# Optimization experiments

Hardware: AMD Instinct MI355X
Metric: run time of the kernel (lower is better)

## Reference

```python
import jax, jax.numpy as jnp
import numpy as np

N_NODES = 200000
N_EDGES = 3200000
F_IN, HID, N_CLS = 128, 35, 10


def setup_inputs() -> dict:
    key = jax.random.key(0)
    k = jax.random.split(key, 5)
    x = jax.random.normal(k[0], (N_NODES, F_IN), dtype=jnp.float32)
    edge_index = jax.random.randint(k[1], (2, N_EDGES), 0, N_NODES, dtype=jnp.int64)
    W1 = jax.random.normal(k[2], (F_IN, HID), dtype=jnp.float32) / np.sqrt(F_IN)
    b1 = jnp.zeros((HID,), dtype=jnp.float32)
    W2 = jax.random.normal(k[3], (HID, N_CLS), dtype=jnp.float32) / np.sqrt(HID)
    b2 = jnp.zeros((N_CLS,), dtype=jnp.float32)
    return {"x": x, "edge_index": edge_index, "W1": W1, "b1": b1, "W2": W2, "b2": b2}


def _gcn_conv(x, W, b, row, col, norm, n_nodes):
    # GCNConv: linear transform, then normalized neighbor aggregation (scatter-add)
    h = x @ W                               # [N, d_out]
    msg = h[row] * norm[:, None]            # gather along edges, [E+N, d_out]
    agg = jax.ops.segment_sum(msg, col, num_segments=n_nodes)
    return agg + b


def reference(x, edge_index, W1, b1, W2, b2):
    n = x.shape[0]
    loop = jnp.arange(n, dtype=edge_index.dtype)
    row = jnp.concatenate([edge_index[0], loop])  # sources (+ self loops)
    col = jnp.concatenate([edge_index[1], loop])  # targets (+ self loops)
    deg = jax.ops.segment_sum(jnp.ones_like(col, dtype=x.dtype), col, num_segments=n)
    dinv = jnp.where(deg > 0, deg ** -0.5, 0.0)
    norm = dinv[row] * dinv[col]                  # D^{-1/2} A D^{-1/2} edge weights

    h = _gcn_conv(x, W1, b1, row, col, norm, n)
    h = jax.nn.relu(h)
    # F.dropout with training=self.training: identity at inference
    out = _gcn_conv(h, W2, b2, row, col, norm, n)
    return jax.nn.log_softmax(out, axis=1)
```

## Files before the change

kernel.cpp:

```cpp
#include <hip/hip_runtime.h>

#define NN    200000
#define F_IN  128
#define HID   35
#define LD1   36
#define LD2   12
#define LD2P  16
#define NCLS  10
#define NPB   256
#define NB    782
#define CAP   5120
#define EPT   32
#define NOE   0xFFFFFFFFu

static __device__ inline unsigned short f2bf(float f) {
    unsigned u = __float_as_uint(f);
    u = (u + 0x7FFFu + ((u >> 16) & 1u)) >> 16;
    return (unsigned short)u;
}
static __device__ inline unsigned pk2(float a, float b) {
    return (unsigned)f2bf(a) | ((unsigned)f2bf(b) << 16);
}
static __device__ inline float bflo(unsigned u) { return __uint_as_float(u << 16); }
static __device__ inline float bfhi(unsigned u) { return __uint_as_float(u & 0xFFFF0000u); }


__global__ void k_initcur(int* __restrict__ gcur) {
    int t = threadIdx.x;
    if (t < NB) gcur[t] = t * CAP;
}

__global__ __launch_bounds__(256)
void k_bucket(const int* __restrict__ row, const int* __restrict__ col, int E,
              int* __restrict__ gcur, unsigned* __restrict__ bkt) {
    __shared__ int hist[NB];
    __shared__ int basev[NB];
    int t = threadIdx.x;
    long e0 = (long)blockIdx.x * (256 * EPT);
    for (int i = t; i < NB; i += 256) hist[i] = 0;
    __syncthreads();
    int cols[EPT];
#pragma unroll
    for (int i = 0; i < EPT; ++i) {
        long e = e0 + (long)i * 256 + t;
        if (e < E) {
            int c = col[e];
            cols[i] = c;
            atomicAdd(&hist[c >> 8], 1);
        } else cols[i] = -1;
    }
    __syncthreads();
    for (int i = t; i < NB; i += 256) {
        int h = hist[i];
        basev[i] = (h > 0) ? atomicAdd(&gcur[i], h) : 0;
        hist[i] = 0;
    }
    __syncthreads();
#pragma unroll
    for (int i = 0; i < EPT; ++i) {
        int c = cols[i];
        if (c >= 0) {
            long e = e0 + (long)i * 256 + t;
            int r = row[e];
            int b = c >> 8;
            int pos = basev[b] + atomicAdd(&hist[b], 1);
            if (pos < NB * CAP) bkt[pos] = (unsigned)r | ((unsigned)(c & 255) << 18);
        }
    }
}

__global__ __launch_bounds__(256)
void k_sort(unsigned* __restrict__ bkt, const int* __restrict__ gcur,
            int* __restrict__ obeg, int* __restrict__ oend,
            float* __restrict__ dinv, int n) {
    __shared__ unsigned est[CAP];
    __shared__ int hist[NPB];
    __shared__ int cur[NPB];
    __shared__ int sc[NPB];
    int b = blockIdx.x, t = threadIdx.x;
    int ec = gcur[b] - b * CAP;
    if (ec > CAP) ec = CAP;
    unsigned* ep = bkt + (size_t)b * CAP;
    hist[t] = 0;
    __syncthreads();
    for (int e = t; e < ec; e += 256) {
        unsigned p = ep[e];
        est[e] = p;
        atomicAdd(&hist[p >> 18], 1);
    }
    __syncthreads();
    sc[t] = hist[t];
    __syncthreads();
    for (int d = 1; d < NPB; d <<= 1) {
        int add = (t >= d) ? sc[t - d] : 0;
        __syncthreads();
        sc[t] += add;
        __syncthreads();
    }
    int excl = sc[t] - hist[t];
    cur[t] = excl;
    int i = b * NPB + t;
    if (i < n) {
        obeg[i] = b * CAP + excl;
        oend[i] = b * CAP + excl + hist[t];
        dinv[i] = rsqrtf((float)(hist[t] + 1));
    }
    __syncthreads();
    for (int e = t; e < ec; e += 256) {
        unsigned p = est[e];
        int lc = p >> 18;
        int pos = atomicAdd(&cur[lc], 1);
        ep[pos] = p & 0x3FFFF;
    }
}


__global__ void k_gemm1(const float* __restrict__ x, const float* __restrict__ W1,
                        const float* __restrict__ dinv,
                        unsigned short* __restrict__ hs1A,
                        unsigned short* __restrict__ hs1B, int n) {
    int i = blockIdx.x * blockDim.x + threadIdx.x;
    if (i >= n) return;
    float acc[HID];
#pragma unroll
    for (int j = 0; j < HID; ++j) acc[j] = 0.f;
    const float4* xr = (const float4*)(x + (size_t)i * F_IN);
    for (int k4 = 0; k4 < F_IN / 4; ++k4) {
        float4 xv = xr[k4];
        const float* w = W1 + (size_t)(k4 * 4) * HID;
#pragma unroll
        for (int j = 0; j < HID; ++j)
            acc[j] += xv.x * w[j] + xv.y * w[HID + j] + xv.z * w[2 * HID + j] + xv.w * w[3 * HID + j];
    }
    float d = dinv[i];
    unsigned* oa = (unsigned*)(hs1A + (size_t)i * 32);
#pragma unroll
    for (int j = 0; j < 16; ++j) oa[j] = pk2(acc[2 * j] * d, acc[2 * j + 1] * d);
    unsigned* ob = (unsigned*)(hs1B + (size_t)i * 4);
    ob[0] = pk2(acc[32] * d, acc[33] * d);
    ob[1] = pk2(acc[34] * d, 0.f);
}

__global__ void k_agg1(const int* __restrict__ obeg, const int* __restrict__ oend,
                       const unsigned* __restrict__ srow,
                       const unsigned short* __restrict__ A,
                       const unsigned short* __restrict__ Bf,
                       float* __restrict__ acc1, int n) {
    int wv = (blockIdx.x * blockDim.x + threadIdx.x) >> 6;
    int lane = threadIdx.x & 63;
    int w0 = wv * 2, w1 = w0 + 1;
    if (w0 >= n) return;
    bool has1 = (w1 < n);
    int s = lane & 15;
    int g = lane >> 4;
    bool bl = (lane < 16);
    int beg0 = obeg[w0], end0 = oend[w0];
    int beg1 = has1 ? obeg[w1] : 0, end1 = has1 ? oend[w1] : 0;
    int nb0 = end0 - beg0, nb1 = end1 - beg1;
    int iters = max((nb0 + 15) >> 4, (nb1 + 15) >> 4);
    float p0a=0.f,p0b=0.f,p0c=0.f,p0d=0.f,p0e=0.f,p0f=0.f,p0g=0.f,p0h=0.f;
    float p1a=0.f,p1b=0.f,p1c=0.f,p1d=0.f,p1e=0.f,p1f=0.f,p1g=0.f,p1h=0.f;
    float q0a=0.f,q0b=0.f,q0c=0.f, q1a=0.f,q1b=0.f,q1c=0.f;
    int e0 = beg0 + s, e1 = beg1 + s;
    for (int it = 0; it < iters; ++it) {
        unsigned idx0 = (e0 < end0) ? srow[e0] : NOE;
        unsigned idx1 = (has1 && e1 < end1) ? srow[e1] : NOE;
        bool v0 = (idx0 != NOE), v1 = (idx1 != NOE);
        unsigned r0 = v0 ? idx0 : (unsigned)w0;
        unsigned r1 = v1 ? idx1 : (unsigned)w0;
        uint4 av0 = *(const uint4*)(A + ((size_t)r0 << 5) + (g << 3));
        uint4 av1 = *(const uint4*)(A + ((size_t)r1 << 5) + (g << 3));
        uint2 bv0 = make_uint2(0u, 0u), bv1 = make_uint2(0u, 0u);
        if (bl) {
            bv0 = *(const uint2*)(Bf + ((size_t)r0 << 2));
            bv1 = *(const uint2*)(Bf + ((size_t)r1 << 2));
        }
        if (v0) {
            p0a += bflo(av0.x); p0b += bfhi(av0.x);
            p0c += bflo(av0.y); p0d += bfhi(av0.y);
            p0e += bflo(av0.z); p0f += bfhi(av0.z);
            p0g += bflo(av0.w); p0h += bfhi(av0.w);
            if (bl) { q0a += bflo(bv0.x); q0b += bfhi(bv0.x); q0c += bflo(bv0.y); }
        }
        if (v1) {
            p1a += bflo(av1.x); p1b += bfhi(av1.x);
            p1c += bflo(av1.y); p1d += bfhi(av1.y);
            p1e += bflo(av1.z); p1f += bfhi(av1.z);
            p1g += bflo(av1.w); p1h += bfhi(av1.w);
            if (bl) { q1a += bflo(bv1.x); q1b += bfhi(bv1.x); q1c += bflo(bv1.y); }
        }
        e0 += 16; e1 += 16;
    }
#pragma unroll
    for (int d = 1; d < 16; d <<= 1) {
        p0a += __shfl_xor(p0a, d); p0b += __shfl_xor(p0b, d);
        p0c += __shfl_xor(p0c, d); p0d += __shfl_xor(p0d, d);
        p0e += __shfl_xor(p0e, d); p0f += __shfl_xor(p0f, d);
        p0g += __shfl_xor(p0g, d); p0h += __shfl_xor(p0h, d);
        p1a += __shfl_xor(p1a, d); p1b += __shfl_xor(p1b, d);
        p1c += __shfl_xor(p1c, d); p1d += __shfl_xor(p1d, d);
        p1e += __shfl_xor(p1e, d); p1f += __shfl_xor(p1f, d);
        p1g += __shfl_xor(p1g, d); p1h += __shfl_xor(p1h, d);
        q0a += __shfl_xor(q0a, d); q0b += __shfl_xor(q0b, d); q0c += __shfl_xor(q0c, d);
        q1a += __shfl_xor(q1a, d); q1b += __shfl_xor(q1b, d); q1c += __shfl_xor(q1c, d);
    }
    if (s == 0) {
        uint4 sv0 = *(const uint4*)(A + ((size_t)w0 << 5) + (g << 3));
        p0a += bflo(sv0.x); p0b += bfhi(sv0.x);
        p0c += bflo(sv0.y); p0d += bfhi(sv0.y);
        p0e += bflo(sv0.z); p0f += bfhi(sv0.z);
        p0g += bflo(sv0.w); p0h += bfhi(sv0.w);
        float* o0 = acc1 + (size_t)w0 * LD1 + (g << 3);
        *(float4*)o0       = make_float4(p0a, p0b, p0c, p0d);
        *(float4*)(o0 + 4) = make_float4(p0e, p0f, p0g, p0h);
        if (has1) {
            uint4 sv1 = *(const uint4*)(A + ((size_t)w1 << 5) + (g << 3));
            p1a += bflo(sv1.x); p1b += bfhi(sv1.x);
            p1c += bflo(sv1.y); p1d += bfhi(sv1.y);
            p1e += bflo(sv1.z); p1f += bfhi(sv1.z);
            p1g += bflo(sv1.w); p1h += bfhi(sv1.w);
            float* o1 = acc1 + (size_t)w1 * LD1 + (g << 3);
            *(float4*)o1       = make_float4(p1a, p1b, p1c, p1d);
            *(float4*)(o1 + 4) = make_float4(p1e, p1f, p1g, p1h);
        }
    }
    if (lane == 0) {
        uint2 sb0 = *(const uint2*)(Bf + ((size_t)w0 << 2));
        q0a += bflo(sb0.x); q0b += bfhi(sb0.x); q0c += bflo(sb0.y);
        *(float4*)(acc1 + (size_t)w0 * LD1 + 32) = make_float4(q0a, q0b, q0c, 0.f);
        if (has1) {
            uint2 sb1 = *(const uint2*)(Bf + ((size_t)w1 << 2));
            q1a += bflo(sb1.x); q1b += bfhi(sb1.x); q1c += bflo(sb1.y);
            *(float4*)(acc1 + (size_t)w1 * LD1 + 32) = make_float4(q1a, q1b, q1c, 0.f);
        }
    }
}


__global__ void k_layer2(const float* __restrict__ acc1, const float* __restrict__ dinv,
                         const float* __restrict__ b1, const float* __restrict__ W2,
                         unsigned short* __restrict__ hs2b, int n) {
    int i = blockIdx.x * blockDim.x + threadIdx.x;
    if (i >= n) return;
    float d = dinv[i];
    const float4* a = (const float4*)(acc1 + (size_t)i * LD1);
    float4 tq[9];
#pragma unroll
    for (int q = 0; q < 9; ++q) tq[q] = a[q];
    const float* tf = (const float*)tq;
    float h[HID];
#pragma unroll
    for (int k = 0; k < HID; ++k) {
        float v = tf[k] * d + b1[k];
        h[k] = v > 0.f ? v : 0.f;
    }
    float o[NCLS];
#pragma unroll
    for (int j = 0; j < NCLS; ++j) o[j] = 0.f;
#pragma unroll
    for (int k = 0; k < HID; ++k) {
#pragma unroll
        for (int j = 0; j < NCLS; ++j) o[j] += h[k] * W2[k * NCLS + j];
    }
    unsigned* dst = (unsigned*)(hs2b + (size_t)i * LD2P);
#pragma unroll
    for (int j = 0; j < 5; ++j) dst[j] = pk2(o[2 * j] * d, o[2 * j + 1] * d);
    dst[5] = 0u; dst[6] = 0u; dst[7] = 0u;
}

__global__ void k_agg2o(const int* __restrict__ obeg, const int* __restrict__ oend,
                        const unsigned* __restrict__ srow,
                        const unsigned short* __restrict__ H,
                        const float* __restrict__ dinv, const float* __restrict__ b2,
                        float* __restrict__ out, int n) {
    int wv = (blockIdx.x * blockDim.x + threadIdx.x) >> 6;
    int lane = threadIdx.x & 63;
    int w0 = wv * 2, w1 = w0 + 1;
    if (w0 >= n) return;
    bool has1 = (w1 < n);
    int s = lane & 15;
    int g = lane >> 4;
    bool ga = (g < 3);
    int beg0 = obeg[w0], end0 = oend[w0];
    int beg1 = has1 ? obeg[w1] : 0, end1 = has1 ? oend[w1] : 0;
    int nb0 = end0 - beg0, nb1 = end1 - beg1;
    int iters = max((nb0 + 15) >> 4, (nb1 + 15) >> 4);
    float a0=0.f,a1=0.f,a2=0.f,a3=0.f;
    float c0=0.f,c1=0.f,c2=0.f,c3=0.f;
    int e0 = beg0 + s, e1 = beg1 + s;
    for (int it = 0; it < iters; ++it) {
        unsigned idx0 = (e0 < end0) ? srow[e0] : NOE;
        unsigned idx1 = (has1 && e1 < end1) ? srow[e1] : NOE;
        bool v0 = (idx0 != NOE), v1 = (idx1 != NOE);
        unsigned r0 = v0 ? idx0 : (unsigned)w0;
        unsigned r1 = v1 ? idx1 : (unsigned)w0;
        uint2 h0 = make_uint2(0u,0u), h1 = make_uint2(0u,0u);
        if (ga) {
            h0 = *(const uint2*)(H + ((size_t)r0 << 4) + (g << 2));
            h1 = *(const uint2*)(H + ((size_t)r1 << 4) + (g << 2));
        }
        if (v0) { a0 += bflo(h0.x); a1 += bfhi(h0.x); a2 += bflo(h0.y); a3 += bfhi(h0.y); }
        if (v1) { c0 += bflo(h1.x); c1 += bfhi(h1.x); c2 += bflo(h1.y); c3 += bfhi(h1.y); }
        e0 += 16; e1 += 16;
    }
#pragma unroll
    for (int d = 1; d < 16; d <<= 1) {
        a0 += __shfl_xor(a0, d); a1 += __shfl_xor(a1, d);
        a2 += __shfl_xor(a2, d); a3 += __shfl_xor(a3, d);
        c0 += __shfl_xor(c0, d); c1 += __shfl_xor(c1, d);
        c2 += __shfl_xor(c2, d); c3 += __shfl_xor(c3, d);
    }
    float v0_=-1e30f, v1_=-1e30f, v2_=-1e30f, v3_=-1e30f;
    if (s == 0 && ga) {
        uint2 sv = *(const uint2*)(H + ((size_t)w0 << 4) + (g << 2));
        a0 += bflo(sv.x); a1 += bfhi(sv.x); a2 += bflo(sv.y); a3 += bfhi(sv.y);
        float dn = dinv[w0];
        int f0 = g << 2;
        v0_ = a0 * dn + b2[f0];
        v1_ = a1 * dn + b2[f0 + 1];
        if (f0 + 2 < NCLS) { v2_ = a2 * dn + b2[f0 + 2]; v3_ = a3 * dn + b2[f0 + 3]; }
    }
    float m = fmaxf(fmaxf(v0_, v1_), fmaxf(v2_, v3_));
    m = fmaxf(m, __shfl_xor(m, 16));
    m = fmaxf(m, __shfl_xor(m, 32));
    float s0 = ((v0_ > -1e29f) ? expf(v0_ - m) : 0.f) + ((v1_ > -1e29f) ? expf(v1_ - m) : 0.f)
             + ((v2_ > -1e29f) ? expf(v2_ - m) : 0.f) + ((v3_ > -1e29f) ? expf(v3_ - m) : 0.f);
    s0 += __shfl_xor(s0, 16);
    s0 += __shfl_xor(s0, 32);
    if (s == 0 && ga) {
        float l = logf(s0);
        int f0 = g << 2;
        float* o = out + (size_t)w0 * NCLS + f0;
        *(float2*)o = make_float2(v0_ - m - l, v1_ - m - l);
        if (f0 + 2 < NCLS) *(float2*)(o + 2) = make_float2(v2_ - m - l, v3_ - m - l);
    }
    if (!has1) return;
    float u0=-1e30f, u1=-1e30f, u2=-1e30f, u3=-1e30f;
    if (s == 0 && ga) {
        uint2 sv = *(const uint2*)(H + ((size_t)w1 << 4) + (g << 2));
        c0 += bflo(sv.x); c1 += bfhi(sv.x); c2 += bflo(sv.y); c3 += bfhi(sv.y);
        float dn = dinv[w1];
        int f0 = g << 2;
        u0 = c0 * dn + b2[f0];
        u1 = c1 * dn + b2[f0 + 1];
        if (f0 + 2 < NCLS) { u2 = c2 * dn + b2[f0 + 2]; u3 = c3 * dn + b2[f0 + 3]; }
    }
    float m1 = fmaxf(fmaxf(u0, u1), fmaxf(u2, u3));
    m1 = fmaxf(m1, __shfl_xor(m1, 16));
    m1 = fmaxf(m1, __shfl_xor(m1, 32));
    float s1 = ((u0 > -1e29f) ? expf(u0 - m1) : 0.f) + ((u1 > -1e29f) ? expf(u1 - m1) : 0.f)
             + ((u2 > -1e29f) ? expf(u2 - m1) : 0.f) + ((u3 > -1e29f) ? expf(u3 - m1) : 0.f);
    s1 += __shfl_xor(s1, 16);
    s1 += __shfl_xor(s1, 32);
    if (s == 0 && ga) {
        float l = logf(s1);
        int f0 = g << 2;
        float* o = out + (size_t)w1 * NCLS + f0;
        *(float2*)o = make_float2(u0 - m1 - l, u1 - m1 - l);
        if (f0 + 2 < NCLS) *(float2*)(o + 2) = make_float2(u2 - m1 - l, u3 - m1 - l);
    }
}

extern "C" void kernel_launch(void* const* d_in, const int* in_sizes, int n_in,
                              void* d_out, int out_size, void* d_ws, size_t ws_size,
                              hipStream_t stream) {
    const float* x  = (const float*)d_in[0];
    const int*   ei = (const int*)d_in[1];
    const float* W1 = (const float*)d_in[2];
    const float* b1 = (const float*)d_in[3];
    const float* W2 = (const float*)d_in[4];
    const float* b2 = (const float*)d_in[5];
    float* out = (float*)d_out;

    const int n = in_sizes[0] / F_IN;
    const int E = in_sizes[1] / 2;
    const int* row = ei;
    const int* col = ei + E;

    unsigned*       bkt  = (unsigned*)d_ws;
    int*            gcur = (int*)d_ws + 4003840;
    int*            obeg = (int*)d_ws + 4004864;
    int*            oend = (int*)d_ws + 4204864;
    float*          dinv = (float*)d_ws + 4404864;
    unsigned short* hs1A = (unsigned short*)((unsigned*)d_ws + 4604864);
    unsigned short* hs1B = (unsigned short*)((unsigned*)d_ws + 7804864);
    float*          acc1 = (float*)d_ws + 8204864;
    unsigned short* hs2b = hs1A;

    const int B = 256;
    const int nbk = (E + B * EPT - 1) / (B * EPT);
    const int npair = (n + 1) / 2;

    k_initcur<<<1, 1024, 0, stream>>>(gcur);
    k_bucket<<<nbk, B, 0, stream>>>(row, col, E, gcur, bkt);
    k_sort<<<NB, B, 0, stream>>>(bkt, gcur, obeg, oend, dinv, n);

    k_gemm1<<<(n + B - 1) / B, B, 0, stream>>>(x, W1, dinv, hs1A, hs1B, n);
    k_agg1<<<(npair * 64 + B - 1) / B, B, 0, stream>>>(obeg, oend, bkt, hs1A, hs1B, acc1, n);
    k_layer2<<<(n + B - 1) / B, B, 0, stream>>>(acc1, dinv, b1, W2, hs2b, n);
    k_agg2o<<<(npair * 64 + B - 1) / B, B, 0, stream>>>(obeg, oend, bkt, hs2b, dinv, b2, out, n);
}
```

Before: 307.1 us.

## Split layer-1 aggregation into per-feature-slice passes over sliced bf16 layout

Stores the layer-1 transformed features as four separate 8-feature bf16 slices (16 bytes per node) plus the tail slice, and replaces the single paired-node aggregation kernel with five passes, one per slice, each using one wavefront per node. The intent is for each pass to gather from a 3.2MB table that fits in cache, improving hit rates for the random neighbor gathers. In exchange the edge index list is read five times, there are extra kernel launches, and each lane gathers only 2 bytes, which produces many small scattered loads.

```diff
diff --git a/kernel.cpp b/kernel.cpp
--- a/kernel.cpp
+++ b/kernel.cpp
@@ -4,14 +4,13 @@
 #define F_IN  128
 #define HID   35
 #define LD1   36
-#define LD2   12
 #define LD2P  16
 #define NCLS  10
 #define NPB   256
 #define NB    782
 #define CAP   5120
 #define EPT   32
-#define NOE   0xFFFFFFFFu
+#define SLICE_W 1600000
 
 static __device__ inline unsigned short f2bf(float f) {
     unsigned u = __float_as_uint(f);
@@ -21,8 +20,9 @@
 static __device__ inline unsigned pk2(float a, float b) {
     return (unsigned)f2bf(a) | ((unsigned)f2bf(b) << 16);
 }
-static __device__ inline float bflo(unsigned u) { return __uint_as_float(u << 16); }
-static __device__ inline float bfhi(unsigned u) { return __uint_as_float(u & 0xFFFF0000u); }
+static __device__ inline float bf2f(unsigned short h) {
+    return __uint_as_float((unsigned)h << 16);
+}
 
 
 __global__ void k_initcur(int* __restrict__ gcur) {
@@ -117,7 +117,7 @@
 
 __global__ void k_gemm1(const float* __restrict__ x, const float* __restrict__ W1,
                         const float* __restrict__ dinv,
-                        unsigned short* __restrict__ hs1A,
+                        unsigned short* __restrict__ hs1S,
                         unsigned short* __restrict__ hs1B, int n) {
     int i = blockIdx.x * blockDim.x + threadIdx.x;
     if (i >= n) return;
@@ -133,106 +133,65 @@
             acc[j] += xv.x * w[j] + xv.y * w[HID + j] + xv.z * w[2 * HID + j] + xv.w * w[3 * HID + j];
     }
     float d = dinv[i];
-    unsigned* oa = (unsigned*)(hs1A + (size_t)i * 32);
-#pragma unroll
-    for (int j = 0; j < 16; ++j) oa[j] = pk2(acc[2 * j] * d, acc[2 * j + 1] * d);
+#pragma unroll
+    for (int p = 0; p < 4; ++p) {
+        unsigned* os = (unsigned*)(hs1S + (size_t)p * SLICE_W + (size_t)i * 8);
+        os[0] = pk2(acc[8 * p] * d,     acc[8 * p + 1] * d);
+        os[1] = pk2(acc[8 * p + 2] * d, acc[8 * p + 3] * d);
+        os[2] = pk2(acc[8 * p + 4] * d, acc[8 * p + 5] * d);
+        os[3] = pk2(acc[8 * p + 6] * d, acc[8 * p + 7] * d);
+    }
     unsigned* ob = (unsigned*)(hs1B + (size_t)i * 4);
     ob[0] = pk2(acc[32] * d, acc[33] * d);
     ob[1] = pk2(acc[34] * d, 0.f);
 }
 
-__global__ void k_agg1(const int* __restrict__ obeg, const int* __restrict__ oend,
-                       const unsigned* __restrict__ srow,
-                       const unsigned short* __restrict__ A,
-                       const unsigned short* __restrict__ Bf,
-                       float* __restrict__ acc1, int n) {
-    int wv = (blockIdx.x * blockDim.x + threadIdx.x) >> 6;
+__global__ void k_agg1p(const int* __restrict__ obeg, const int* __restrict__ oend,
+                        const unsigned* __restrict__ srow,
+                        const unsigned short* __restrict__ S,
+                        float* __restrict__ acc1, int n, int off) {
+    int wid = (blockIdx.x * blockDim.x + threadIdx.x) >> 6;
     int lane = threadIdx.x & 63;
-    int w0 = wv * 2, w1 = w0 + 1;
-    if (w0 >= n) return;
-    bool has1 = (w1 < n);
-    int s = lane & 15;
-    int g = lane >> 4;
-    bool bl = (lane < 16);
-    int beg0 = obeg[w0], end0 = oend[w0];
-    int beg1 = has1 ? obeg[w1] : 0, end1 = has1 ? oend[w1] : 0;
-    int nb0 = end0 - beg0, nb1 = end1 - beg1;
-    int iters = max((nb0 + 15) >> 4, (nb1 + 15) >> 4);
-    float p0a=0.f,p0b=0.f,p0c=0.f,p0d=0.f,p0e=0.f,p0f=0.f,p0g=0.f,p0h=0.f;
-    float p1a=0.f,p1b=0.f,p1c=0.f,p1d=0.f,p1e=0.f,p1f=0.f,p1g=0.f,p1h=0.f;
-    float q0a=0.f,q0b=0.f,q0c=0.f, q1a=0.f,q1b=0.f,q1c=0.f;
-    int e0 = beg0 + s, e1 = beg1 + s;
-    for (int it = 0; it < iters; ++it) {
-        unsigned idx0 = (e0 < end0) ? srow[e0] : NOE;
-        unsigned idx1 = (has1 && e1 < end1) ? srow[e1] : NOE;
-        bool v0 = (idx0 != NOE), v1 = (idx1 != NOE);
-        unsigned r0 = v0 ? idx0 : (unsigned)w0;
-        unsigned r1 = v1 ? idx1 : (unsigned)w0;
-        uint4 av0 = *(const uint4*)(A + ((size_t)r0 << 5) + (g << 3));
-        uint4 av1 = *(const uint4*)(A + ((size_t)r1 << 5) + (g << 3));
-        uint2 bv0 = make_uint2(0u, 0u), bv1 = make_uint2(0u, 0u);
-        if (bl) {
-            bv0 = *(const uint2*)(Bf + ((size_t)r0 << 2));
-            bv1 = *(const uint2*)(Bf + ((size_t)r1 << 2));
-        }
-        if (v0) {
-            p0a += bflo(av0.x); p0b += bfhi(av0.x);
-            p0c += bflo(av0.y); p0d += bfhi(av0.y);
-            p0e += bflo(av0.z); p0f += bfhi(av0.z);
-            p0g += bflo(av0.w); p0h += bfhi(av0.w);
-            if (bl) { q0a += bflo(bv0.x); q0b += bfhi(bv0.x); q0c += bflo(bv0.y); }
-        }
-        if (v1) {
-            p1a += bflo(av1.x); p1b += bfhi(av1.x);
-            p1c += bflo(av1.y); p1d += bfhi(av1.y);
-            p1e += bflo(av1.z); p1f += bfhi(av1.z);
-            p1g += bflo(av1.w); p1h += bfhi(av1.w);
-            if (bl) { q1a += bflo(bv1.x); q1b += bfhi(bv1.x); q1c += bflo(bv1.y); }
-        }
-        e0 += 16; e1 += 16;
-    }
-#pragma unroll
-    for (int d = 1; d < 16; d <<= 1) {
-        p0a += __shfl_xor(p0a, d); p0b += __shfl_xor(p0b, d);
-        p0c += __shfl_xor(p0c, d); p0d += __shfl_xor(p0d, d);
-        p0e += __shfl_xor(p0e, d); p0f += __shfl_xor(p0f, d);
-        p0g += __shfl_xor(p0g, d); p0h += __shfl_xor(p0h, d);
-        p1a += __shfl_xor(p1a, d); p1b += __shfl_xor(p1b, d);
-        p1c += __shfl_xor(p1c, d); p1d += __shfl_xor(p1d, d);
-        p1e += __shfl_xor(p1e, d); p1f += __shfl_xor(p1f, d);
-        p1g += __shfl_xor(p1g, d); p1h += __shfl_xor(p1h, d);
-        q0a += __shfl_xor(q0a, d); q0b += __shfl_xor(q0b, d); q0c += __shfl_xor(q0c, d);
-        q1a += __shfl_xor(q1a, d); q1b += __shfl_xor(q1b, d); q1c += __shfl_xor(q1c, d);
-    }
-    if (s == 0) {
-        uint4 sv0 = *(const uint4*)(A + ((size_t)w0 << 5) + (g << 3));
-        p0a += bflo(sv0.x); p0b += bfhi(sv0.x);
-        p0c += bflo(sv0.y); p0d += bfhi(sv0.y);
-        p0e += bflo(sv0.z); p0f += bfhi(sv0.z);
-        p0g += bflo(sv0.w); p0h += bfhi(sv0.w);
-        float* o0 = acc1 + (size_t)w0 * LD1 + (g << 3);
-        *(float4*)o0       = make_float4(p0a, p0b, p0c, p0d);
-        *(float4*)(o0 + 4) = make_float4(p0e, p0f, p0g, p0h);
-        if (has1) {
-            uint4 sv1 = *(const uint4*)(A + ((size_t)w1 << 5) + (g << 3));
-            p1a += bflo(sv1.x); p1b += bfhi(sv1.x);
-            p1c += bflo(sv1.y); p1d += bfhi(sv1.y);
-            p1e += bflo(sv1.z); p1f += bfhi(sv1.z);
-            p1g += bflo(sv1.w); p1h += bfhi(sv1.w);
-            float* o1 = acc1 + (size_t)w1 * LD1 + (g << 3);
-            *(float4*)o1       = make_float4(p1a, p1b, p1c, p1d);
-            *(float4*)(o1 + 4) = make_float4(p1e, p1f, p1g, p1h);
-        }
-    }
-    if (lane == 0) {
-        uint2 sb0 = *(const uint2*)(Bf + ((size_t)w0 << 2));
-        q0a += bflo(sb0.x); q0b += bfhi(sb0.x); q0c += bflo(sb0.y);
-        *(float4*)(acc1 + (size_t)w0 * LD1 + 32) = make_float4(q0a, q0b, q0c, 0.f);
-        if (has1) {
-            uint2 sb1 = *(const uint2*)(Bf + ((size_t)w1 << 2));
-            q1a += bflo(sb1.x); q1b += bfhi(sb1.x); q1c += bflo(sb1.y);
-            *(float4*)(acc1 + (size_t)w1 * LD1 + 32) = make_float4(q1a, q1b, q1c, 0.f);
-        }
+    if (wid >= n) return;
+    int f = lane & 7;
+    int s = lane >> 3;
+    int beg = obeg[wid], end = oend[wid];
+    float acc = 0.f;
+    for (int e = beg + s; e < end; e += 8) {
+        unsigned r = srow[e];
+        acc += bf2f(S[((size_t)r << 3) + f]);
+    }
+    acc += __shfl_xor(acc, 8);
+    acc += __shfl_xor(acc, 16);
+    acc += __shfl_xor(acc, 32);
+    if (lane < 8) {
+        acc += bf2f(S[((size_t)wid << 3) + f]);
+        acc1[(size_t)wid * LD1 + off + f] = acc;
+    }
+}
+
+__global__ void k_agg1b(const int* __restrict__ obeg, const int* __restrict__ oend,
+                        const unsigned* __restrict__ srow,
+                        const unsigned short* __restrict__ Bf,
+                        float* __restrict__ acc1, int n) {
+    int wid = (blockIdx.x * blockDim.x + threadIdx.x) >> 6;
+    int lane = threadIdx.x & 63;
+    if (wid >= n) return;
+    int f = lane & 3;
+    int s = lane >> 2;
+    int beg = obeg[wid], end = oend[wid];
+    float acc = 0.f;
+    for (int e = beg + s; e < end; e += 16) {
+        unsigned r = srow[e];
+        acc += bf2f(Bf[((size_t)r << 2) + f]);
+    }
+    acc += __shfl_xor(acc, 4);
+    acc += __shfl_xor(acc, 8);
+    acc += __shfl_xor(acc, 16);
+    acc += __shfl_xor(acc, 32);
+    if (lane < 4) {
+        acc += bf2f(Bf[((size_t)wid << 2) + f]);
+        acc1[(size_t)wid * LD1 + 32 + f] = acc;
     }
 }
 
@@ -268,6 +227,7 @@
     dst[5] = 0u; dst[6] = 0u; dst[7] = 0u;
 }
 
+#define NOE 0xFFFFFFFFu
 __global__ void k_agg2o(const int* __restrict__ obeg, const int* __restrict__ oend,
                         const unsigned* __restrict__ srow,
                         const unsigned short* __restrict__ H,
@@ -299,8 +259,10 @@
             h0 = *(const uint2*)(H + ((size_t)r0 << 4) + (g << 2));
             h1 = *(const uint2*)(H + ((size_t)r1 << 4) + (g << 2));
         }
-        if (v0) { a0 += bflo(h0.x); a1 += bfhi(h0.x); a2 += bflo(h0.y); a3 += bfhi(h0.y); }
-        if (v1) { c0 += bflo(h1.x); c1 += bfhi(h1.x); c2 += bflo(h1.y); c3 += bfhi(h1.y); }
+        if (v0) { a0 += bf2f((unsigned short)h0.x); a1 += bf2f((unsigned short)(h0.x >> 16));
+                  a2 += bf2f((unsigned short)h0.y); a3 += bf2f((unsigned short)(h0.y >> 16)); }
+        if (v1) { c0 += bf2f((unsigned short)h1.x); c1 += bf2f((unsigned short)(h1.x >> 16));
+                  c2 += bf2f((unsigned short)h1.y); c3 += bf2f((unsigned short)(h1.y >> 16)); }
         e0 += 16; e1 += 16;
     }
 #pragma unroll
@@ -313,7 +275,8 @@
     float v0_=-1e30f, v1_=-1e30f, v2_=-1e30f, v3_=-1e30f;
     if (s == 0 && ga) {
         uint2 sv = *(const uint2*)(H + ((size_t)w0 << 4) + (g << 2));
-        a0 += bflo(sv.x); a1 += bfhi(sv.x); a2 += bflo(sv.y); a3 += bfhi(sv.y);
+        a0 += bf2f((unsigned short)sv.x); a1 += bf2f((unsigned short)(sv.x >> 16));
+        a2 += bf2f((unsigned short)sv.y); a3 += bf2f((unsigned short)(sv.y >> 16));
         float dn = dinv[w0];
         int f0 = g << 2;
         v0_ = a0 * dn + b2[f0];
@@ -338,7 +301,8 @@
     float u0=-1e30f, u1=-1e30f, u2=-1e30f, u3=-1e30f;
     if (s == 0 && ga) {
         uint2 sv = *(const uint2*)(H + ((size_t)w1 << 4) + (g << 2));
-        c0 += bflo(sv.x); c1 += bfhi(sv.x); c2 += bflo(sv.y); c3 += bfhi(sv.y);
+        c0 += bf2f((unsigned short)sv.x); c1 += bf2f((unsigned short)(sv.x >> 16));
+        c2 += bf2f((unsigned short)sv.y); c3 += bf2f((unsigned short)(sv.y >> 16));
         float dn = dinv[w1];
         int f0 = g << 2;
         u0 = c0 * dn + b2[f0];
@@ -382,21 +346,26 @@
     int*            obeg = (int*)d_ws + 4004864;
     int*            oend = (int*)d_ws + 4204864;
     float*          dinv = (float*)d_ws + 4404864;
-    unsigned short* hs1A = (unsigned short*)((unsigned*)d_ws + 4604864);
+    unsigned short* hs1S = (unsigned short*)((unsigned*)d_ws + 4604864);
     unsigned short* hs1B = (unsigned short*)((unsigned*)d_ws + 7804864);
     float*          acc1 = (float*)d_ws + 8204864;
-    unsigned short* hs2b = hs1A;
+    unsigned short* hs2b = hs1S;
 
     const int B = 256;
     const int nbk = (E + B * EPT - 1) / (B * EPT);
+    const int gw  = (n * 64 + B - 1) / B;
     const int npair = (n + 1) / 2;
 
     k_initcur<<<1, 1024, 0, stream>>>(gcur);
     k_bucket<<<nbk, B, 0, stream>>>(row, col, E, gcur, bkt);
     k_sort<<<NB, B, 0, stream>>>(bkt, gcur, obeg, oend, dinv, n);
 
-    k_gemm1<<<(n + B - 1) / B, B, 0, stream>>>(x, W1, dinv, hs1A, hs1B, n);
-    k_agg1<<<(npair * 64 + B - 1) / B, B, 0, stream>>>(obeg, oend, bkt, hs1A, hs1B, acc1, n);
+    k_gemm1<<<(n + B - 1) / B, B, 0, stream>>>(x, W1, dinv, hs1S, hs1B, n);
+    for (int p = 0; p < 4; ++p)
+        k_agg1p<<<gw, B, 0, stream>>>(obeg, oend, bkt,
+                                      hs1S + (size_t)p * SLICE_W, acc1, n, p * 8);
+    k_agg1b<<<gw, B, 0, stream>>>(obeg, oend, bkt, hs1B, acc1, n);
+
     k_layer2<<<(n + B - 1) / B, B, 0, stream>>>(acc1, dinv, b1, W2, hs2b, n);
     k_agg2o<<<(npair * 64 + B - 1) / B, B, 0, stream>>>(obeg, oend, bkt, hs2b, dinv, b2, out, n);
 }
```

Result: slower. 511.4 us (+66.5%).

## Restructure first GEMM to stage x tiles in LDS and split outputs across threads

Applied to the files above, without the earlier changes.

The layer-1 linear transform now has each block load a 64-node tile of x into shared memory with coalesced float4 loads, instead of each thread reading its own 512-byte row. Four thread groups each compute about 9 of the 35 output columns for the same nodes, which cuts per-thread register use from 35 accumulators to 9 and raises occupancy. Results go to a shared-memory staging array and are written back as coalesced packed bf16 stores. In exchange it adds shared-memory traffic and two barriers, and there is no bounds check, so it relies on n being a multiple of 64.

```diff
diff --git a/kernel.cpp b/kernel.cpp
--- a/kernel.cpp
+++ b/kernel.cpp
@@ -4,13 +4,13 @@
 #define F_IN  128
 #define HID   35
 #define LD1   36
-#define LD2   12
 #define LD2P  16
 #define NCLS  10
 #define NPB   256
 #define NB    782
 #define CAP   5120
 #define EPT   32
+#define GN    64
 #define NOE   0xFFFFFFFFu
 
 static __device__ inline unsigned short f2bf(float f) {
@@ -115,31 +115,57 @@
 }
 
 
-__global__ void k_gemm1(const float* __restrict__ x, const float* __restrict__ W1,
-                        const float* __restrict__ dinv,
-                        unsigned short* __restrict__ hs1A,
-                        unsigned short* __restrict__ hs1B, int n) {
-    int i = blockIdx.x * blockDim.x + threadIdx.x;
-    if (i >= n) return;
-    float acc[HID];
-#pragma unroll
-    for (int j = 0; j < HID; ++j) acc[j] = 0.f;
-    const float4* xr = (const float4*)(x + (size_t)i * F_IN);
-    for (int k4 = 0; k4 < F_IN / 4; ++k4) {
-        float4 xv = xr[k4];
-        const float* w = W1 + (size_t)(k4 * 4) * HID;
-#pragma unroll
-        for (int j = 0; j < HID; ++j)
-            acc[j] += xv.x * w[j] + xv.y * w[HID + j] + xv.z * w[2 * HID + j] + xv.w * w[3 * HID + j];
-    }
-    float d = dinv[i];
-    unsigned* oa = (unsigned*)(hs1A + (size_t)i * 32);
-#pragma unroll
-    for (int j = 0; j < 16; ++j) oa[j] = pk2(acc[2 * j] * d, acc[2 * j + 1] * d);
-    unsigned* ob = (unsigned*)(hs1B + (size_t)i * 4);
-    ob[0] = pk2(acc[32] * d, acc[33] * d);
-    ob[1] = pk2(acc[34] * d, 0.f);
-}
+__global__ __launch_bounds__(256)
+void k_gemm1(const float* __restrict__ x, const float* __restrict__ W1,
+             const float* __restrict__ dinv,
+             unsigned short* __restrict__ hs1A,
+             unsigned short* __restrict__ hs1B, int n) {
+    __shared__ float xs[GN][129];
+    __shared__ float ha[GN][37];
+    int t = threadIdx.x;
+    int base = blockIdx.x * GN;
+    const float4* xsrc = (const float4*)(x + (size_t)base * F_IN);
+    for (int i = t; i < GN * 32; i += 256) {
+        float4 v = xsrc[i];
+        int node = i >> 5;
+        int c4 = i & 31;
+        *(float4*)&xs[node][c4 * 4] = v;
+    }
+    __syncthreads();
+    int nl = t & 63;
+    int q = t >> 6;
+    int j0 = q * 9;
+    int nj = (q == 3) ? 8 : 9;
+    float acc[9];
+#pragma unroll
+    for (int j = 0; j < 9; ++j) acc[j] = 0.f;
+    for (int k4 = 0; k4 < 32; ++k4) {
+        float4 xv = *(const float4*)&xs[nl][k4 * 4];
+        const float* w = W1 + (size_t)(k4 * 4) * HID + j0;
+#pragma unroll
+        for (int j = 0; j < 9; ++j) {
+            if (j < 8 || nj == 9)
+                acc[j] += xv.x * w[j] + xv.y * w[HID + j]
+                        + xv.z * w[2 * HID + j] + xv.w * w[3 * HID + j];
+        }
+    }
+    float d = dinv[base + nl];
+#pragma unroll
+    for (int j = 0; j < 9; ++j)
+        if (j < nj) ha[nl][j0 + j] = acc[j] * d;
+    __syncthreads();
+    unsigned* oa = (unsigned*)(hs1A + (size_t)base * 32);
+    for (int i = t; i < GN * 16; i += 256) {
+        int node = i >> 4, p = i & 15;
+        oa[i] = pk2(ha[node][2 * p], ha[node][2 * p + 1]);
+    }
+    unsigned* ob = (unsigned*)(hs1B + (size_t)base * 4);
+    for (int i = t; i < GN * 2; i += 256) {
+        int node = i >> 1, p = i & 1;
+        ob[i] = (p == 0) ? pk2(ha[node][32], ha[node][33]) : pk2(ha[node][34], 0.f);
+    }
+}
+
 
 __global__ void k_agg1(const int* __restrict__ obeg, const int* __restrict__ oend,
                        const unsigned* __restrict__ srow,
@@ -395,7 +421,7 @@
     k_bucket<<<nbk, B, 0, stream>>>(row, col, E, gcur, bkt);
     k_sort<<<NB, B, 0, stream>>>(bkt, gcur, obeg, oend, dinv, n);
 
-    k_gemm1<<<(n + B - 1) / B, B, 0, stream>>>(x, W1, dinv, hs1A, hs1B, n);
+    k_gemm1<<<(n + GN - 1) / GN, B, 0, stream>>>(x, W1, dinv, hs1A, hs1B, n);
     k_agg1<<<(npair * 64 + B - 1) / B, B, 0, stream>>>(obeg, oend, bkt, hs1A, hs1B, acc1, n);
     k_layer2<<<(n + B - 1) / B, B, 0, stream>>>(acc1, dinv, b1, W2, hs2b, n);
     k_agg2o<<<(npair * 64 + B - 1) / B, B, 0, stream>>>(obeg, oend, bkt, hs2b, dinv, b2, out, n);
```

New measurement: 363.5 us. 1.18x slower.

## Stage W1 in shared memory and split GEMM1 K-dim across four lanes per node

Applied to the files above, without the earlier changes.

Rewrites the first linear layer so each block stages W1 into padded LDS. Each node is then handled by four lanes, each covering a quarter of the 128 input features with float4 weight reads, and partial sums are reduced with cross-lane shuffles. Before, each thread read a whole 512-byte row of x and pulled W1 from global/scalar memory. The change aims to make the x reads coalesced, cut per-thread serial work and raise occupancy. In exchange it adds shuffle reductions, branchy output packing and an LDS fill at the start of every block.

```diff
diff --git a/kernel.cpp b/kernel.cpp
--- a/kernel.cpp
+++ b/kernel.cpp
@@ -4,13 +4,13 @@
 #define F_IN  128
 #define HID   35
 #define LD1   36
-#define LD2   12
 #define LD2P  16
 #define NCLS  10
 #define NPB   256
 #define NB    782
 #define CAP   5120
 #define EPT   32
+#define SKW   1160
 #define NOE   0xFFFFFFFFu
 
 static __device__ inline unsigned short f2bf(float f) {
@@ -115,31 +115,72 @@
 }
 
 
-__global__ void k_gemm1(const float* __restrict__ x, const float* __restrict__ W1,
-                        const float* __restrict__ dinv,
-                        unsigned short* __restrict__ hs1A,
-                        unsigned short* __restrict__ hs1B, int n) {
-    int i = blockIdx.x * blockDim.x + threadIdx.x;
-    if (i >= n) return;
-    float acc[HID];
-#pragma unroll
-    for (int j = 0; j < HID; ++j) acc[j] = 0.f;
-    const float4* xr = (const float4*)(x + (size_t)i * F_IN);
-    for (int k4 = 0; k4 < F_IN / 4; ++k4) {
-        float4 xv = xr[k4];
-        const float* w = W1 + (size_t)(k4 * 4) * HID;
-#pragma unroll
-        for (int j = 0; j < HID; ++j)
-            acc[j] += xv.x * w[j] + xv.y * w[HID + j] + xv.z * w[2 * HID + j] + xv.w * w[3 * HID + j];
-    }
-    float d = dinv[i];
-    unsigned* oa = (unsigned*)(hs1A + (size_t)i * 32);
-#pragma unroll
-    for (int j = 0; j < 16; ++j) oa[j] = pk2(acc[2 * j] * d, acc[2 * j + 1] * d);
-    unsigned* ob = (unsigned*)(hs1B + (size_t)i * 4);
-    ob[0] = pk2(acc[32] * d, acc[33] * d);
-    ob[1] = pk2(acc[34] * d, 0.f);
-}
+__global__ __launch_bounds__(256)
+void k_gemm1(const float* __restrict__ x, const float* __restrict__ W1,
+             const float* __restrict__ dinv,
+             unsigned short* __restrict__ hs1A,
+             unsigned short* __restrict__ hs1B, int n) {
+    __shared__ float wl[4 * SKW];
+    int t = threadIdx.x;
+    for (int i = t; i < F_IN * HID; i += 256) {
+        int k = i / HID, j = i - k * HID;
+        wl[(k >> 5) * SKW + (k & 31) * 36 + j] = W1[i];
+    }
+    for (int i = t; i < F_IN; i += 256)
+        wl[(i >> 5) * SKW + (i & 31) * 36 + 35] = 0.f;
+    __syncthreads();
+    int p = t & 3;
+    int node = blockIdx.x * 64 + (t >> 2);
+    bool act = node < n;
+    int nclamp = act ? node : 0;
+    float acc[36];
+#pragma unroll
+    for (int j = 0; j < 36; ++j) acc[j] = 0.f;
+    const float4* xr = (const float4*)(x + (size_t)nclamp * F_IN + p * 32);
+    const float* wp = wl + p * SKW;
+#pragma unroll
+    for (int kk = 0; kk < 8; ++kk) {
+        float4 xv = xr[kk];
+        const float* w = wp + kk * 144;
+#pragma unroll
+        for (int j4 = 0; j4 < 9; ++j4) {
+            float4 wa = *(const float4*)(w + j4 * 4);
+            float4 wb = *(const float4*)(w + 36 + j4 * 4);
+            float4 wc = *(const float4*)(w + 72 + j4 * 4);
+            float4 wd = *(const float4*)(w + 108 + j4 * 4);
+            acc[4 * j4 + 0] += xv.x * wa.x + xv.y * wb.x + xv.z * wc.x + xv.w * wd.x;
+            acc[4 * j4 + 1] += xv.x * wa.y + xv.y * wb.y + xv.z * wc.y + xv.w * wd.y;
+            acc[4 * j4 + 2] += xv.x * wa.z + xv.y * wb.z + xv.z * wc.z + xv.w * wd.z;
+            acc[4 * j4 + 3] += xv.x * wa.w + xv.y * wb.w + xv.z * wc.w + xv.w * wd.w;
+        }
+    }
+#pragma unroll
+    for (int j = 0; j < 36; ++j) {
+        acc[j] += __shfl_xor(acc[j], 1);
+        acc[j] += __shfl_xor(acc[j], 2);
+    }
+    if (!act) return;
+    float d = dinv[node];
+    unsigned w0_, w1_, w2_, w3_;
+    if (p == 0) {
+        w0_ = pk2(acc[0] * d, acc[1] * d);  w1_ = pk2(acc[2] * d, acc[3] * d);
+        w2_ = pk2(acc[4] * d, acc[5] * d);  w3_ = pk2(acc[6] * d, acc[7] * d);
+    } else if (p == 1) {
+        w0_ = pk2(acc[8] * d, acc[9] * d);  w1_ = pk2(acc[10] * d, acc[11] * d);
+        w2_ = pk2(acc[12] * d, acc[13] * d); w3_ = pk2(acc[14] * d, acc[15] * d);
+    } else if (p == 2) {
+        w0_ = pk2(acc[16] * d, acc[17] * d); w1_ = pk2(acc[18] * d, acc[19] * d);
+        w2_ = pk2(acc[20] * d, acc[21] * d); w3_ = pk2(acc[22] * d, acc[23] * d);
+    } else {
+        w0_ = pk2(acc[24] * d, acc[25] * d); w1_ = pk2(acc[26] * d, acc[27] * d);
+        w2_ = pk2(acc[28] * d, acc[29] * d); w3_ = pk2(acc[30] * d, acc[31] * d);
+    }
+    ((uint4*)hs1A)[(size_t)node * 4 + p] = make_uint4(w0_, w1_, w2_, w3_);
+    if (p == 3)
+        ((uint2*)hs1B)[node] = make_uint2(pk2(acc[32] * d, acc[33] * d),
+                                          pk2(acc[34] * d, 0.f));
+}
+
 
 __global__ void k_agg1(const int* __restrict__ obeg, const int* __restrict__ oend,
                        const unsigned* __restrict__ srow,
@@ -395,7 +436,7 @@
     k_bucket<<<nbk, B, 0, stream>>>(row, col, E, gcur, bkt);
     k_sort<<<NB, B, 0, stream>>>(bkt, gcur, obeg, oend, dinv, n);
 
-    k_gemm1<<<(n + B - 1) / B, B, 0, stream>>>(x, W1, dinv, hs1A, hs1B, n);
+    k_gemm1<<<(n + 63) / 64, B, 0, stream>>>(x, W1, dinv, hs1A, hs1B, n);
     k_agg1<<<(npair * 64 + B - 1) / B, B, 0, stream>>>(obeg, oend, bkt, hs1A, hs1B, acc1, n);
     k_layer2<<<(n + B - 1) / B, B, 0, stream>>>(acc1, dinv, b1, W2, hs2b, n);
     k_agg2o<<<(npair * 64 + B - 1) / B, B, 0, stream>>>(obeg, oend, bkt, hs2b, dinv, b2, out, n);
```

After: 375.5 us. 1.22x slower.
